# Optimization experiments

Hardware: AMD Instinct MI355X
Metric: run time of the kernel (lower is better)

Reference implementation:

```python
import jax, jax.numpy as jnp
import numpy as np

ANNEAL_T_START = 5.0
T_END = 1.0


def setup_inputs() -> dict:
    key = jax.random.key(0)
    ks = jax.random.split(key, 8)
    B, V, H, CD, WID = 8192, 1024, 128, 16, 64
    return {
        "cond": jax.random.normal(ks[0], (B, CD), jnp.float32),
        "W": 0.01 * jax.random.normal(ks[1], (V, H), jnp.float32),
        "b": 0.01 * jax.random.normal(ks[2], (V,), jnp.float32),
        "c": 0.01 * jax.random.normal(ks[3], (H,), jnp.float32),
        "fc1_w": jax.random.normal(ks[4], (WID, CD), jnp.float32) / np.float32(np.sqrt(CD)),
        "fc1_b": jnp.zeros((WID,), jnp.float32),
        "fc2_w": jax.random.normal(ks[5], (2 * (V + H), WID), jnp.float32) / np.float32(np.sqrt(WID)),
        "fc2_b": jnp.zeros((2 * (V + H),), jnp.float32),
        "falloff": jnp.float32(1.0),
        "steps": 16,
    }


def _bern(key, p):
    # Bernoulli sample as float of same dtype as p.
    return (jax.random.uniform(key, p.shape, p.dtype) < p).astype(p.dtype)


def reference(cond, W, b, c, fc1_w, fc1_b, fc2_w, fc2_b, falloff, steps):
    V, H = W.shape
    B = cond.shape[0]
    dtype = W.dtype

    # Conditioner: FiLM-style modulation of visible/hidden biases.
    x = jnp.tanh(cond @ fc1_w.T + fc1_b)
    x = x @ fc2_w.T + fc2_b  # [B, 2*(V+H)]
    gamma_b = x[:, :V]
    beta_b = x[:, V:2 * V]
    gamma_c = x[:, 2 * V:2 * V + H]
    beta_c = x[:, 2 * V + H:]
    b_mod = (1.0 + gamma_b) * b + beta_b  # [B, V]
    c_mod = (1.0 + gamma_c) * c + beta_c  # [B, H]
    bsum = jnp.sum(b_mod, axis=-1)  # [B], constant across steps

    # Annealing temperature schedule (sigmoid falloff).
    t = jnp.arange(steps, dtype=dtype)
    s = 1.0 / (1.0 + jnp.exp(falloff * (t - steps / 2.0)))
    temps = T_END + (ANNEAL_T_START - T_END) * s  # [steps]

    base = jax.random.key(42)
    v0 = _bern(jax.random.fold_in(base, 2 ** 20), jnp.full((B, V), 0.5, dtype))
    s0_0 = jnp.ones((B, 1), dtype)

    def flip(v, s0):
        return s0 * v + (1.0 - s0) * (1.0 - v)

    def step(carry, xs):
        v, s0 = carry
        i, T = xs
        k1, k2, k3 = jax.random.split(jax.random.fold_in(base, i), 3)
        v_eff = flip(v, s0)
        p_h = jax.nn.sigmoid((v_eff @ W + c_mod) / T)  # [B, H]
        h = _bern(k1, p_h)
        a = h @ W.T  # [B, V]
        vb = jnp.sum(v * b_mod, axis=-1)
        va = jnp.sum(v * a, axis=-1)
        dE = -bsum - jnp.sum(a, axis=-1) + 2.0 * vb + 2.0 * va  # [B]
        p_s0 = jax.nn.sigmoid(dE / T)
        s0n = _bern(k2, p_s0)[:, None]  # [B, 1]
        p_v = jax.nn.sigmoid((a + b_mod) / T)
        v_samp = _bern(k3, p_v)
        v_next = flip(v_samp, s0n)
        return (v_next, s0n), None

    (v, _), _ = jax.lax.scan(
        step, (v0, s0_0), (jnp.arange(steps, dtype=jnp.int32), temps)
    )
    return v
```

## Files before the change

### kernel.cpp

```cpp
#include <hip/hip_runtime.h>
#include <stdint.h>

#pragma clang fp contract(off)

#define B_ 8192
#define V_ 1024
#define H_ 128
#define CD_ 16
#define WID_ 64
#define NOUT_ 2304
#define STEPS_ 16

typedef float f32x2 __attribute__((ext_vector_type(2)));

__device__ __forceinline__ void pkfma(f32x2& acc, f32x2 wv, f32x2 bf2) {
  asm("v_pk_fma_f32 %0, %1, %2, %0" : "+v"(acc) : "v"(wv), "v"(bf2));
}

__host__ __device__ __forceinline__ void tf2x32(uint32_t k0, uint32_t k1,
                                                uint32_t x0, uint32_t x1,
                                                uint32_t* o0, uint32_t* o1) {
  uint32_t ks2 = k0 ^ k1 ^ 0x1BD11BDAu;
#define RL_(v, d) (((v) << (d)) | ((v) >> (32 - (d))))
#define RND_(a) { x0 += x1; x1 = RL_(x1, a); x1 ^= x0; }
  x0 += k0; x1 += k1;
  RND_(13) RND_(15) RND_(26) RND_(6)
  x0 += k1; x1 += ks2 + 1u;
  RND_(17) RND_(29) RND_(16) RND_(24)
  x0 += ks2; x1 += k0 + 2u;
  RND_(13) RND_(15) RND_(26) RND_(6)
  x0 += k0; x1 += k1 + 3u;
  RND_(17) RND_(29) RND_(16) RND_(24)
  x0 += k1; x1 += ks2 + 4u;
  RND_(13) RND_(15) RND_(26) RND_(6)
  x0 += ks2; x1 += k0 + 5u;
#undef RND_
#undef RL_
  *o0 = x0; *o1 = x1;
}

struct Keys { uint32_t a[6]; };

__device__ __forceinline__ uint32_t draw_bits(uint32_t ka, uint32_t kb, uint32_t j) {
  uint32_t x0, x1;
  tf2x32(ka, kb, 0u, j, &x0, &x1);
  return x0 ^ x1;
}

__device__ __forceinline__ float bits_to_u(uint32_t bits) {
  return __fsub_rn(__uint_as_float((bits >> 9) | 0x3f800000u), 1.0f);
}

__device__ __forceinline__ float exp_a(float x) {
  float xc = fminf(fmaxf(x, -88.3762626647949f), 88.3762626647950f);
  float fx = floorf(__fadd_rn(__fmul_rn(xc, 1.44269504088896341f), 0.5f));
  float xr = __fsub_rn(xc, __fmul_rn(0.693359375f, fx));
  xr = __fsub_rn(xr, __fmul_rn(-2.12194440e-4f, fx));
  float zz = __fmul_rn(xr, xr);
  float y = 1.9875691500E-4f;
  y = __fadd_rn(__fmul_rn(y, xr), 1.3981999507E-3f);
  y = __fadd_rn(__fmul_rn(y, xr), 8.3334519073E-3f);
  y = __fadd_rn(__fmul_rn(y, xr), 4.1665795894E-2f);
  y = __fadd_rn(__fmul_rn(y, xr), 1.6666665459E-1f);
  y = __fadd_rn(__fmul_rn(y, xr), 5.0000001201E-1f);
  y = __fadd_rn(__fmul_rn(y, zz), xr);
  y = __fadd_rn(y, 1.0f);
  int n = (int)fx;
  float sc = __int_as_float((n + 127) << 23);
  return __fmul_rn(y, sc);
}

__device__ __forceinline__ float tanh_a(float xin) {
  float x = fmaxf(fminf(xin, 7.90531110763549805f), -7.90531110763549805f);
  float x2 = __fmul_rn(x, x);
  float p = __fadd_rn(__fmul_rn(x2, -2.76076847742355e-16f), 2.00018790482477e-13f);
  p = __fadd_rn(__fmul_rn(x2, p), -8.60467152213735e-11f);
  p = __fadd_rn(__fmul_rn(x2, p), 5.12229709037114e-08f);
  p = __fadd_rn(__fmul_rn(x2, p), 1.48572235717979e-05f);
  p = __fadd_rn(__fmul_rn(x2, p), 6.37261928875436e-04f);
  p = __fadd_rn(__fmul_rn(x2, p), 4.89352455891786e-03f);
  p = __fmul_rn(x, p);
  float q = __fadd_rn(__fmul_rn(x2, 1.19825839466702e-06f), 1.18534705686654e-04f);
  q = __fadd_rn(__fmul_rn(x2, q), 2.26843463243900e-03f);
  q = __fadd_rn(__fmul_rn(x2, q), 4.89352518554385e-03f);
  float r = p / q;
  if (fabsf(xin) < 0.0004f) r = xin;
  return r;
}

__device__ __forceinline__ float sigmoid_a(float z) {
  float e = exp_a(-z);
  return 1.0f / __fadd_rn(1.0f, e);
}

__global__ void k_transpose(const float* __restrict__ W, float* __restrict__ WT,
                            const float* __restrict__ fc2w, float* __restrict__ fc2T) {
  int i = blockIdx.x * blockDim.x + threadIdx.x;
  if (i < V_ * H_) { int v = i / H_, h = i % H_; WT[h * V_ + v] = W[i]; }
  if (i < NOUT_ * WID_) { int j = i / WID_, w = i % WID_; fc2T[w * NOUT_ + j] = fc2w[i]; }
}

__global__ void k_temps(const float* __restrict__ falloff, float* __restrict__ temps) {
  int t = threadIdx.x;
  if (t < 16) {
    float arg = __fmul_rn(*falloff, __fsub_rn((float)t, 8.0f));
    float e = exp_a(arg);
    float s = 1.0f / __fadd_rn(1.0f, e);
    temps[t] = __fadd_rn(1.0f, __fmul_rn(4.0f, s));
  }
}

__global__ void k_mlp1(const float* __restrict__ cond, const float* __restrict__ fc1w,
                       const float* __restrict__ fc1b, float* __restrict__ xout) {
  int idx = blockIdx.x * blockDim.x + threadIdx.x;
  if (idx >= B_ * WID_) return;
  int row = idx >> 6, w = idx & 63;
  float acc = 0.0f;
  for (int k = 0; k < CD_; k++) acc = __fmaf_rn(cond[row * CD_ + k], fc1w[w * CD_ + k], acc);
  float z = __fadd_rn(acc, fc1b[w]);
  xout[idx] = tanh_a(z);
}

__global__ __launch_bounds__(128) void k_mlp2b(const float* __restrict__ xmlp,
                       const float* __restrict__ fc2T, const float* __restrict__ fc2b,
                       const float* __restrict__ bvec, float* __restrict__ b_mod) {
  __shared__ float xs[32][WID_];
  int jbase = blockIdx.x * 128;
  int r0 = blockIdx.y * 32;
  int tid = threadIdx.x;
  for (int t = tid; t < 32 * WID_; t += 128)
    xs[t >> 6][t & 63] = xmlp[(r0 + (t >> 6)) * WID_ + (t & 63)];
  __syncthreads();
  int j = jbase + tid;
  float accg[32], accb[32];
#pragma unroll
  for (int r = 0; r < 32; r++) { accg[r] = 0.0f; accb[r] = 0.0f; }
  for (int w = 0; w < WID_; w++) {
    float fg = fc2T[w * NOUT_ + j];
    float fb = fc2T[w * NOUT_ + 1024 + j];
#pragma unroll
    for (int r = 0; r < 32; r++) {
      float xv = xs[r][w];
      accg[r] = __fmaf_rn(xv, fg, accg[r]);
      accb[r] = __fmaf_rn(xv, fb, accb[r]);
    }
  }
  float bj = bvec[j];
  float biasg = fc2b[j], biasb = fc2b[1024 + j];
#pragma unroll
  for (int r = 0; r < 32; r++) {
    float g = __fadd_rn(accg[r], biasg);
    float bb = __fadd_rn(accb[r], biasb);
    float t1 = __fadd_rn(1.0f, g);
    b_mod[(r0 + r) * V_ + j] = __fadd_rn(__fmul_rn(t1, bj), bb);
  }
}

__global__ __launch_bounds__(128) void k_mlp2c(const float* __restrict__ xmlp,
                       const float* __restrict__ fc2T, const float* __restrict__ fc2b,
                       const float* __restrict__ cvec, float* __restrict__ c_mod) {
  __shared__ float xs[32][WID_];
  int r0 = blockIdx.y * 32;
  int tid = threadIdx.x;
  for (int t = tid; t < 32 * WID_; t += 128)
    xs[t >> 6][t & 63] = xmlp[(r0 + (t >> 6)) * WID_ + (t & 63)];
  __syncthreads();
  float accg[32], accb[32];
#pragma unroll
  for (int r = 0; r < 32; r++) { accg[r] = 0.0f; accb[r] = 0.0f; }
  for (int w = 0; w < WID_; w++) {
    float fg = fc2T[w * NOUT_ + 2048 + tid];
    float fb = fc2T[w * NOUT_ + 2176 + tid];
#pragma unroll
    for (int r = 0; r < 32; r++) {
      float xv = xs[r][w];
      accg[r] = __fmaf_rn(xv, fg, accg[r]);
      accb[r] = __fmaf_rn(xv, fb, accb[r]);
    }
  }
  float cj = cvec[tid];
  float biasg = fc2b[2048 + tid], biasb = fc2b[2176 + tid];
#pragma unroll
  for (int r = 0; r < 32; r++) {
    float g = __fadd_rn(accg[r], biasg);
    float bb = __fadd_rn(accb[r], biasb);
    float t1 = __fadd_rn(1.0f, g);
    c_mod[(r0 + r) * H_ + tid] = __fadd_rn(__fmul_rn(t1, cj), bb);
  }
}

__global__ __launch_bounds__(64) void k_bsum(const float* __restrict__ b_mod,
                                             float* __restrict__ bsum) {
  int row = blockIdx.x * 64 + threadIdx.x;
  const float4* bp = (const float4*)(b_mod + (size_t)row * V_);
  float acc = 0.0f;
  for (int c = 0; c < 32; c++) {
    float4 Bv[8];
#pragma unroll
    for (int q = 0; q < 8; q++) Bv[q] = bp[c * 8 + q];
#pragma unroll
    for (int q = 0; q < 8; q++) {
      acc = __fadd_rn(acc, Bv[q].x);
      acc = __fadd_rn(acc, Bv[q].y);
      acc = __fadd_rn(acc, Bv[q].z);
      acc = __fadd_rn(acc, Bv[q].w);
    }
  }
  bsum[row] = acc;
}

__global__ void k_v0(float* __restrict__ vout, uint32_t* __restrict__ v_bits,
                     float* __restrict__ s0, uint32_t kva, uint32_t kvb) {
  int idx = blockIdx.x * blockDim.x + threadIdx.x;
  int row = idx >> 10, col = idx & 1023;
  uint32_t bits = draw_bits(kva, kvb, (uint32_t)idx);
  float u = bits_to_u(bits);
  float v = (u < 0.5f) ? 1.0f : 0.0f;
  vout[idx] = v;
  unsigned long long m = __ballot(v == 1.0f);
  if ((threadIdx.x & 63) == 0) {
    v_bits[row * 32 + (col >> 5)] = (uint32_t)m;
    v_bits[row * 32 + (col >> 5) + 1] = (uint32_t)(m >> 32);
  }
  if (col == 0) s0[row] = 1.0f;
}

__global__ __launch_bounds__(256) void k_h(const float* __restrict__ W,
                   const float* __restrict__ c_mod, const uint32_t* __restrict__ v_bits,
                   const float* __restrict__ s0, uint32_t* __restrict__ h_bits,
                   const float* __restrict__ temps, int step, Keys kn) {
  __shared__ float Wt[2][32 * H_];
  __shared__ uint32_t nib[16][32];
  int tid = threadIdx.x;
  int ct = tid & 31;
  int rt = tid >> 5;
  int h0 = ct << 2;
  int row0 = blockIdx.x * 16 + rt * 2;
  float T = temps[step];
  f32x2 acc[2][2];
#pragma unroll
  for (int r = 0; r < 2; r++) { acc[r][0] = f32x2{0.f, 0.f}; acc[r][1] = f32x2{0.f, 0.f}; }
  uint32_t flip[2];
#pragma unroll
  for (int r = 0; r < 2; r++) flip[r] = (s0[row0 + r] == 0.0f) ? 0xFFFFFFFFu : 0u;

  float4 st[4];
  auto stage_load = [&](int tile) {
    const float4* src = (const float4*)(W + (size_t)tile * 32 * H_);
#pragma unroll
    for (int i = 0; i < 4; i++) st[i] = src[tid + i * 256];
  };
  auto stage_store = [&](int bsel) {
    float4* dst = (float4*)&Wt[bsel][0];
#pragma unroll
    for (int i = 0; i < 4; i++) dst[tid + i * 256] = st[i];
  };
  auto compute_tile = [&](int bsel, int tile) {
    uint32_t m[2];
#pragma unroll
    for (int r = 0; r < 2; r++)
      m[r] = __brev(v_bits[(size_t)(row0 + r) * 32 + tile]) ^ flip[r];
#pragma unroll 8
    for (int j = 0; j < 32; j++) {
      float4 wv = *(const float4*)(&Wt[bsel][j * H_ + h0]);
      f32x2 wlo = {wv.x, wv.y};
      f32x2 whi = {wv.z, wv.w};
#pragma unroll
      for (int r = 0; r < 2; r++) {
        uint32_t sm = (uint32_t)((int32_t)m[r] >> 31);
        m[r] <<= 1;
        float bf = __uint_as_float(sm & 0x3f800000u);
        f32x2 b2 = {bf, bf};
        pkfma(acc[r][0], wlo, b2);
        pkfma(acc[r][1], whi, b2);
      }
    }
  };

  stage_load(0);
  stage_store(0);
  __syncthreads();
  for (int t = 0; t < 32; t++) {
    if (t < 31) stage_load(t + 1);
    compute_tile(t & 1, t);
    if (t < 31) stage_store((t + 1) & 1);
    __syncthreads();
  }

#pragma unroll
  for (int r = 0; r < 2; r++) {
    int row = row0 + r;
    float4 cm = *(const float4*)(c_mod + (size_t)row * H_ + h0);
    const float cma[4] = {cm.x, cm.y, cm.z, cm.w};
    const float ac[4] = {acc[r][0][0], acc[r][0][1], acc[r][1][0], acc[r][1][1]};
    uint32_t nb = 0;
#pragma unroll
    for (int e = 0; e < 4; e++) {
      float z = __fadd_rn(ac[e], cma[e]) / T;
      float p = sigmoid_a(z);
      uint32_t b = draw_bits(kn.a[0], kn.a[1], (uint32_t)(row * H_ + h0 + e));
      if (bits_to_u(b) < p) nb |= 1u << e;
    }
    nib[rt * 2 + r][ct] = nb;
  }
  __syncthreads();
  if (tid < 64) {
    int rloc = tid >> 2, wq = tid & 3;
    uint32_t word = 0;
#pragma unroll
    for (int i = 0; i < 8; i++) word |= nib[rloc][wq * 8 + i] << (4 * i);
    h_bits[(size_t)(blockIdx.x * 16 + rloc) * 4 + wq] = word;
  }
}

__global__ __launch_bounds__(256) void k_a(const float* __restrict__ WT,
                   const uint32_t* __restrict__ h_bits, float* __restrict__ a) {
  int tid = threadIdx.x;
  int ct = tid & 63;
  int rt = tid >> 6;
  int v0 = blockIdx.x * 256 + (ct << 2);
  int r0 = blockIdx.y * 32 + rt * 8;
  f32x2 acc[8][2];
#pragma unroll
  for (int r = 0; r < 8; r++) { acc[r][0] = f32x2{0.f, 0.f}; acc[r][1] = f32x2{0.f, 0.f}; }
  uint4 hw[8];
#pragma unroll
  for (int r = 0; r < 8; r++) hw[r] = *(const uint4*)(h_bits + (size_t)(r0 + r) * 4);
  const float* wp0 = WT + v0;

  auto asect = [&](int WW, const uint32_t mwin[8]) {
    uint32_t m[8];
#pragma unroll
    for (int r = 0; r < 8; r++) m[r] = __brev(mwin[r]);
    const float* wp = wp0 + (size_t)(WW * 32) * V_;
    for (int j4 = 0; j4 < 8; j4++) {
#pragma unroll
      for (int jj = 0; jj < 4; jj++) {
        float4 wv = *(const float4*)(wp + (size_t)jj * V_);
        f32x2 wlo = {wv.x, wv.y};
        f32x2 whi = {wv.z, wv.w};
#pragma unroll
        for (int r = 0; r < 8; r++) {
          uint32_t sm = (uint32_t)((int32_t)m[r] >> 31);
          m[r] <<= 1;
          float bf = __uint_as_float(sm & 0x3f800000u);
          f32x2 b2 = {bf, bf};
          pkfma(acc[r][0], wlo, b2);
          pkfma(acc[r][1], whi, b2);
        }
      }
      wp += (size_t)4 * V_;
    }
  };

  {
    uint32_t mw[8];
#pragma unroll
    for (int r = 0; r < 8; r++) mw[r] = hw[r].x;
    asect(0, mw);
#pragma unroll
    for (int r = 0; r < 8; r++) mw[r] = hw[r].y;
    asect(1, mw);
#pragma unroll
    for (int r = 0; r < 8; r++) mw[r] = hw[r].z;
    asect(2, mw);
#pragma unroll
    for (int r = 0; r < 8; r++) mw[r] = hw[r].w;
    asect(3, mw);
  }

#pragma unroll
  for (int r = 0; r < 8; r++) {
    float4 o = make_float4(acc[r][0][0], acc[r][0][1], acc[r][1][0], acc[r][1][1]);
    *(float4*)(a + (size_t)(r0 + r) * V_ + v0) = o;
  }
}

__global__ __launch_bounds__(64) void k_s0(const float* __restrict__ a,
                     const float* __restrict__ b_mod, const float* __restrict__ bsum,
                     const uint32_t* __restrict__ v_bits, float* __restrict__ s0,
                     const float* __restrict__ temps, int step, Keys kn) {
  int row = blockIdx.x * 64 + threadIdx.x;
  const float4* ap = (const float4*)(a + (size_t)row * V_);
  const float4* bp = (const float4*)(b_mod + (size_t)row * V_);
  const uint32_t* vbp = v_bits + row * 32;
  float suma = 0.0f, vb = 0.0f, va = 0.0f;
  float4 A0[8], B0[8], A1[8], B1[8];
  uint32_t m0, m1;

  auto LOADC = [&](int c, float4* A, float4* B, uint32_t& m) {
#pragma unroll
    for (int q = 0; q < 8; q++) { A[q] = ap[c * 8 + q]; B[q] = bp[c * 8 + q]; }
    m = vbp[c];
  };
  auto PROC = [&](const float4* A, const float4* B, uint32_t m) {
#pragma unroll
    for (int q = 0; q < 8; q++) {
      const float ax[4] = {A[q].x, A[q].y, A[q].z, A[q].w};
      const float bx[4] = {B[q].x, B[q].y, B[q].z, B[q].w};
#pragma unroll
      for (int e = 0; e < 4; e++) {
        float bit = (float)((m >> (q * 4 + e)) & 1u);
        suma = __fadd_rn(suma, ax[e]);
        vb = __fmaf_rn(bx[e], bit, vb);
        va = __fmaf_rn(ax[e], bit, va);
      }
    }
  };

  LOADC(0, A0, B0, m0);
  for (int cc = 0; cc < 16; cc++) {
    LOADC(2 * cc + 1, A1, B1, m1);
    PROC(A0, B0, m0);
    if (cc < 15) LOADC(2 * cc + 2, A0, B0, m0);
    PROC(A1, B1, m1);
  }

  float dE = __fsub_rn(-bsum[row], suma);
  dE = __fadd_rn(dE, __fmul_rn(2.0f, vb));
  dE = __fadd_rn(dE, __fmul_rn(2.0f, va));
  float T = temps[step];
  float p = sigmoid_a(dE / T);
  uint32_t bits = draw_bits(kn.a[2], kn.a[3], (uint32_t)row);
  float u = bits_to_u(bits);
  s0[row] = (u < p) ? 1.0f : 0.0f;
}

__global__ void k_v(const float* __restrict__ a, const float* __restrict__ b_mod,
                    const float* __restrict__ s0, float* __restrict__ vout,
                    uint32_t* __restrict__ v_bits, const float* __restrict__ temps, int step,
                    Keys kn) {
  int idx = blockIdx.x * blockDim.x + threadIdx.x;
  int row = idx >> 10, col = idx & 1023;
  float T = temps[step];
  float z = __fadd_rn(a[idx], b_mod[idx]) / T;
  float p = sigmoid_a(z);
  uint32_t bits = draw_bits(kn.a[4], kn.a[5], (uint32_t)idx);
  float u = bits_to_u(bits);
  float vs = (u < p) ? 1.0f : 0.0f;
  float vn = (s0[row] != 0.0f) ? vs : (1.0f - vs);
  vout[idx] = vn;
  unsigned long long m = __ballot(vn == 1.0f);
  if ((threadIdx.x & 63) == 0) {
    v_bits[row * 32 + (col >> 5)] = (uint32_t)m;
    v_bits[row * 32 + (col >> 5) + 1] = (uint32_t)(m >> 32);
  }
}

extern "C" void kernel_launch(void* const* d_in, const int* in_sizes, int n_in,
                              void* d_out, int out_size, void* d_ws, size_t ws_size,
                              hipStream_t stream) {
  const float* cond = (const float*)d_in[0];
  const float* W = (const float*)d_in[1];
  const float* bvec = (const float*)d_in[2];
  const float* cvec = (const float*)d_in[3];
  const float* fc1w = (const float*)d_in[4];
  const float* fc1b = (const float*)d_in[5];
  const float* fc2w = (const float*)d_in[6];
  const float* fc2b = (const float*)d_in[7];
  const float* falloff = (const float*)d_in[8];
  float* out = (float*)d_out;

  char* ws = (char*)d_ws;
  size_t off = 0;
  auto alloc = [&](size_t bytes) { void* p = ws + off; off += (bytes + 255) & ~(size_t)255; return p; };
  float* b_mod = (float*)alloc((size_t)B_ * V_ * 4);
  float* c_mod = (float*)alloc((size_t)B_ * H_ * 4);
  float* abuf  = (float*)alloc((size_t)B_ * V_ * 4);
  float* xmlp  = (float*)alloc((size_t)B_ * WID_ * 4);
  float* bsum  = (float*)alloc((size_t)B_ * 4);
  float* s0    = (float*)alloc((size_t)B_ * 4);
  uint32_t* v_bits = (uint32_t*)alloc((size_t)B_ * 32 * 4);
  uint32_t* h_bits = (uint32_t*)alloc((size_t)B_ * 4 * 4);
  float* WT    = (float*)alloc((size_t)H_ * V_ * 4);
  float* fc2T  = (float*)alloc((size_t)WID_ * NOUT_ * 4);
  float* temps = (float*)alloc(16 * 4);

  uint32_t kva, kvb;
  tf2x32(0u, 42u, 0u, 1048576u, &kva, &kvb);
  Keys kn[16];
  for (int i = 0; i < 16; i++) {
    uint32_t f0, f1;
    tf2x32(0u, 42u, 0u, (uint32_t)i, &f0, &f1);
    uint32_t a0, a1;
    tf2x32(f0, f1, 0u, 0u, &a0, &a1); kn[i].a[0] = a0; kn[i].a[1] = a1;
    tf2x32(f0, f1, 0u, 1u, &a0, &a1); kn[i].a[2] = a0; kn[i].a[3] = a1;
    tf2x32(f0, f1, 0u, 2u, &a0, &a1); kn[i].a[4] = a0; kn[i].a[5] = a1;
  }

  k_transpose<<<(NOUT_ * WID_ + 255) / 256, 256, 0, stream>>>(W, WT, fc2w, fc2T);
  k_temps<<<1, 64, 0, stream>>>(falloff, temps);
  k_mlp1<<<(B_ * WID_) / 256, 256, 0, stream>>>(cond, fc1w, fc1b, xmlp);
  k_mlp2b<<<dim3(8, 256), 128, 0, stream>>>(xmlp, fc2T, fc2b, bvec, b_mod);
  k_mlp2c<<<dim3(1, 256), 128, 0, stream>>>(xmlp, fc2T, fc2b, cvec, c_mod);
  k_bsum<<<B_ / 64, 64, 0, stream>>>(b_mod, bsum);
  k_v0<<<(B_ * V_) / 256, 256, 0, stream>>>(out, v_bits, s0, kva, kvb);

  for (int i = 0; i < STEPS_; i++) {
    k_h<<<B_ / 16, 256, 0, stream>>>(W, c_mod, v_bits, s0, h_bits, temps, i, kn[i]);
    k_a<<<dim3(4, B_ / 32), 256, 0, stream>>>(WT, h_bits, abuf);
    k_s0<<<B_ / 64, 64, 0, stream>>>(abuf, b_mod, bsum, v_bits, s0, temps, i, kn[i]);
    k_v<<<(B_ * V_) / 256, 256, 0, stream>>>(abuf, b_mod, s0, out, v_bits, temps, i, kn[i]);
  }
}
```

Measured before the change: 3.494 ms.

## Stream W from global in k_h and stage k_s0 rows through LDS

```diff
diff --git a/kernel.cpp b/kernel.cpp
--- a/kernel.cpp
+++ b/kernel.cpp
@@ -229,7 +229,6 @@
                    const float* __restrict__ c_mod, const uint32_t* __restrict__ v_bits,
                    const float* __restrict__ s0, uint32_t* __restrict__ h_bits,
                    const float* __restrict__ temps, int step, Keys kn) {
-  __shared__ float Wt[2][32 * H_];
   __shared__ uint32_t nib[16][32];
   int tid = threadIdx.x;
   int ct = tid & 31;
@@ -237,62 +236,66 @@
   int h0 = ct << 2;
   int row0 = blockIdx.x * 16 + rt * 2;
   float T = temps[step];
-  f32x2 acc[2][2];
-#pragma unroll
-  for (int r = 0; r < 2; r++) { acc[r][0] = f32x2{0.f, 0.f}; acc[r][1] = f32x2{0.f, 0.f}; }
-  uint32_t flip[2];
-#pragma unroll
-  for (int r = 0; r < 2; r++) flip[r] = (s0[row0 + r] == 0.0f) ? 0xFFFFFFFFu : 0u;
-
-  float4 st[4];
-  auto stage_load = [&](int tile) {
-    const float4* src = (const float4*)(W + (size_t)tile * 32 * H_);
-#pragma unroll
-    for (int i = 0; i < 4; i++) st[i] = src[tid + i * 256];
+  f32x2 a00 = {0.f, 0.f}, a01 = {0.f, 0.f};
+  f32x2 a10 = {0.f, 0.f}, a11 = {0.f, 0.f};
+  uint32_t flip0 = (s0[row0] == 0.0f) ? 0xFFFFFFFFu : 0u;
+  uint32_t flip1 = (s0[row0 + 1] == 0.0f) ? 0xFFFFFFFFu : 0u;
+  const float* wp = W + h0;
+  const uint4* vb0q = (const uint4*)(v_bits + (size_t)row0 * 32);
+  const uint4* vb1q = (const uint4*)(v_bits + (size_t)(row0 + 1) * 32);
+
+  float4 A[8], Bq[8];
+  uint32_t m0, m1;
+  auto LOADW = [&](float4* d, int kbase) {
+#pragma unroll
+    for (int i = 0; i < 8; i++)
+      d[i] = *(const float4*)(wp + (size_t)(kbase + i) * H_);
   };
-  auto stage_store = [&](int bsel) {
-    float4* dst = (float4*)&Wt[bsel][0];
-#pragma unroll
-    for (int i = 0; i < 4; i++) dst[tid + i * 256] = st[i];
+  auto DO8 = [&](const float4* wv) {
+#pragma unroll
+    for (int j = 0; j < 8; j++) {
+      uint32_t s0m = (uint32_t)((int32_t)m0 >> 31); m0 <<= 1;
+      uint32_t s1m = (uint32_t)((int32_t)m1 >> 31); m1 <<= 1;
+      float bf0 = __uint_as_float(s0m & 0x3f800000u);
+      float bf1 = __uint_as_float(s1m & 0x3f800000u);
+      f32x2 wlo = {wv[j].x, wv[j].y};
+      f32x2 whi = {wv[j].z, wv[j].w};
+      f32x2 b0 = {bf0, bf0};
+      f32x2 b1 = {bf1, bf1};
+      pkfma(a00, wlo, b0); pkfma(a01, whi, b0);
+      pkfma(a10, wlo, b1); pkfma(a11, whi, b1);
+    }
   };
-  auto compute_tile = [&](int bsel, int tile) {
-    uint32_t m[2];
-#pragma unroll
-    for (int r = 0; r < 2; r++)
-      m[r] = __brev(v_bits[(size_t)(row0 + r) * 32 + tile]) ^ flip[r];
-#pragma unroll 8
-    for (int j = 0; j < 32; j++) {
-      float4 wv = *(const float4*)(&Wt[bsel][j * H_ + h0]);
-      f32x2 wlo = {wv.x, wv.y};
-      f32x2 whi = {wv.z, wv.w};
-#pragma unroll
-      for (int r = 0; r < 2; r++) {
-        uint32_t sm = (uint32_t)((int32_t)m[r] >> 31);
-        m[r] <<= 1;
-        float bf = __uint_as_float(sm & 0x3f800000u);
-        f32x2 b2 = {bf, bf};
-        pkfma(acc[r][0], wlo, b2);
-        pkfma(acc[r][1], whi, b2);
-      }
-    }
-  };
-
-  stage_load(0);
-  stage_store(0);
-  __syncthreads();
-  for (int t = 0; t < 32; t++) {
-    if (t < 31) stage_load(t + 1);
-    compute_tile(t & 1, t);
-    if (t < 31) stage_store((t + 1) & 1);
-    __syncthreads();
-  }
-
+
+  uint4 q0 = vb0q[0], q1 = vb1q[0];
+  uint4 q0n, q1n;
+  LOADW(A, 0);
+  for (int kq = 0; kq < 8; kq++) {
+    if (kq < 7) { q0n = vb0q[kq + 1]; q1n = vb1q[kq + 1]; }
+    const uint32_t w0s[4] = {q0.x, q0.y, q0.z, q0.w};
+    const uint32_t w1s[4] = {q1.x, q1.y, q1.z, q1.w};
+#pragma unroll
+    for (int wq = 0; wq < 4; wq++) {
+      int kb = kq * 128 + wq * 32;
+      m0 = __brev(w0s[wq]) ^ flip0;
+      m1 = __brev(w1s[wq]) ^ flip1;
+      LOADW(Bq, kb + 8);  DO8(A);
+      LOADW(A, kb + 16);  DO8(Bq);
+      LOADW(Bq, kb + 24); DO8(A);
+      if (kb + 32 < 1024) LOADW(A, kb + 32);
+      DO8(Bq);
+    }
+    q0 = q0n; q1 = q1n;
+  }
+
+  const f32x2* accs[2][2] = {{&a00, &a01}, {&a10, &a11}};
 #pragma unroll
   for (int r = 0; r < 2; r++) {
     int row = row0 + r;
     float4 cm = *(const float4*)(c_mod + (size_t)row * H_ + h0);
     const float cma[4] = {cm.x, cm.y, cm.z, cm.w};
-    const float ac[4] = {acc[r][0][0], acc[r][0][1], acc[r][1][0], acc[r][1][1]};
+    const float ac[4] = {(*accs[r][0])[0], (*accs[r][0])[1],
+                         (*accs[r][1])[0], (*accs[r][1])[1]};
     uint32_t nb = 0;
 #pragma unroll
     for (int e = 0; e < 4; e++) {
@@ -376,54 +379,68 @@
   }
 }
 
-__global__ __launch_bounds__(64) void k_s0(const float* __restrict__ a,
+__global__ __launch_bounds__(256) void k_s0(const float* __restrict__ a,
                      const float* __restrict__ b_mod, const float* __restrict__ bsum,
                      const uint32_t* __restrict__ v_bits, float* __restrict__ s0,
                      const float* __restrict__ temps, int step, Keys kn) {
-  int row = blockIdx.x * 64 + threadIdx.x;
-  const float4* ap = (const float4*)(a + (size_t)row * V_);
-  const float4* bp = (const float4*)(b_mod + (size_t)row * V_);
-  const uint32_t* vbp = v_bits + row * 32;
+  __shared__ float As[2][16][132];
+  __shared__ float Bs[2][16][132];
+  int tid = threadIdx.x;
+  int r0 = blockIdx.x * 16;
+
+  auto STAGE = [&](int buf, int c) {
+#pragma unroll
+    for (int i = 0; i < 2; i++) {
+      int e = tid + i * 256;
+      int r = e >> 5, c4 = e & 31;
+      float4 av = *(const float4*)(a + (size_t)(r0 + r) * V_ + c * 128 + c4 * 4);
+      float4 bv = *(const float4*)(b_mod + (size_t)(r0 + r) * V_ + c * 128 + c4 * 4);
+      *(float4*)&As[buf][r][c4 * 4] = av;
+      *(float4*)&Bs[buf][r][c4 * 4] = bv;
+    }
+  };
+
   float suma = 0.0f, vb = 0.0f, va = 0.0f;
-  float4 A0[8], B0[8], A1[8], B1[8];
-  uint32_t m0, m1;
-
-  auto LOADC = [&](int c, float4* A, float4* B, uint32_t& m) {
-#pragma unroll
-    for (int q = 0; q < 8; q++) { A[q] = ap[c * 8 + q]; B[q] = bp[c * 8 + q]; }
-    m = vbp[c];
-  };
-  auto PROC = [&](const float4* A, const float4* B, uint32_t m) {
-#pragma unroll
-    for (int q = 0; q < 8; q++) {
-      const float ax[4] = {A[q].x, A[q].y, A[q].z, A[q].w};
-      const float bx[4] = {B[q].x, B[q].y, B[q].z, B[q].w};
-#pragma unroll
-      for (int e = 0; e < 4; e++) {
-        float bit = (float)((m >> (q * 4 + e)) & 1u);
-        suma = __fadd_rn(suma, ax[e]);
-        vb = __fmaf_rn(bx[e], bit, vb);
-        va = __fmaf_rn(ax[e], bit, va);
+  STAGE(0, 0);
+  __syncthreads();
+  for (int c = 0; c < 8; c++) {
+    if (c < 7) STAGE((c + 1) & 1, c + 1);
+    if (tid < 16) {
+      int row = r0 + tid;
+      uint4 mw = *(const uint4*)(v_bits + (size_t)row * 32 + c * 4);
+      const uint32_t mm[4] = {mw.x, mw.y, mw.z, mw.w};
+#pragma unroll
+      for (int w4 = 0; w4 < 4; w4++) {
+        uint32_t m = mm[w4];
+#pragma unroll
+        for (int j4 = 0; j4 < 8; j4++) {
+          float4 av4 = *(const float4*)&As[c & 1][tid][w4 * 32 + j4 * 4];
+          float4 bv4 = *(const float4*)&Bs[c & 1][tid][w4 * 32 + j4 * 4];
+          const float ax[4] = {av4.x, av4.y, av4.z, av4.w};
+          const float bx[4] = {bv4.x, bv4.y, bv4.z, bv4.w};
+#pragma unroll
+          for (int e = 0; e < 4; e++) {
+            float bit = (float)((m >> (j4 * 4 + e)) & 1u);
+            suma = __fadd_rn(suma, ax[e]);
+            vb = __fmaf_rn(bx[e], bit, vb);
+            va = __fmaf_rn(ax[e], bit, va);
+          }
+        }
       }
     }
-  };
-
-  LOADC(0, A0, B0, m0);
-  for (int cc = 0; cc < 16; cc++) {
-    LOADC(2 * cc + 1, A1, B1, m1);
-    PROC(A0, B0, m0);
-    if (cc < 15) LOADC(2 * cc + 2, A0, B0, m0);
-    PROC(A1, B1, m1);
-  }
-
-  float dE = __fsub_rn(-bsum[row], suma);
-  dE = __fadd_rn(dE, __fmul_rn(2.0f, vb));
-  dE = __fadd_rn(dE, __fmul_rn(2.0f, va));
-  float T = temps[step];
-  float p = sigmoid_a(dE / T);
-  uint32_t bits = draw_bits(kn.a[2], kn.a[3], (uint32_t)row);
-  float u = bits_to_u(bits);
-  s0[row] = (u < p) ? 1.0f : 0.0f;
+    __syncthreads();
+  }
+  if (tid < 16) {
+    int row = r0 + tid;
+    float dE = __fsub_rn(-bsum[row], suma);
+    dE = __fadd_rn(dE, __fmul_rn(2.0f, vb));
+    dE = __fadd_rn(dE, __fmul_rn(2.0f, va));
+    float T = temps[step];
+    float p = sigmoid_a(dE / T);
+    uint32_t bits = draw_bits(kn.a[2], kn.a[3], (uint32_t)row);
+    float u = bits_to_u(bits);
+    s0[row] = (u < p) ? 1.0f : 0.0f;
+  }
 }
 
 __global__ void k_v(const float* __restrict__ a, const float* __restrict__ b_mod,
@@ -499,7 +516,7 @@
   for (int i = 0; i < STEPS_; i++) {
     k_h<<<B_ / 16, 256, 0, stream>>>(W, c_mod, v_bits, s0, h_bits, temps, i, kn[i]);
     k_a<<<dim3(4, B_ / 32), 256, 0, stream>>>(WT, h_bits, abuf);
-    k_s0<<<B_ / 64, 64, 0, stream>>>(abuf, b_mod, bsum, v_bits, s0, temps, i, kn[i]);
+    k_s0<<<B_ / 16, 256, 0, stream>>>(abuf, b_mod, bsum, v_bits, s0, temps, i, kn[i]);
     k_v<<<(B_ * V_) / 256, 256, 0, stream>>>(abuf, b_mod, s0, out, v_bits, temps, i, kn[i]);
   }
 }
```

Measured after the change: 2.989 ms. -14.5%, faster.
